# Kernel tuning notes

Measured on AMD Instinct MI355X. Metric: run time of the kernel, lower is better.

The kernel has to match this reference:

```python
import jax, jax.numpy as jnp
import numpy as np

T, B, D = 512, 32, 1024


def setup_inputs() -> dict:
    key = jax.random.key(0)
    kx, kwh, kwx, kwg = jax.random.split(key, 4)
    x = jax.random.normal(kx, (T, B, D), dtype=jnp.float32)
    # W_h: orthogonal init scaled by 0.5
    a = jax.random.normal(kwh, (D, D), dtype=jnp.float32)
    q, r = jnp.linalg.qr(a)
    W_h = 0.5 * q * jnp.sign(jnp.diag(r))[None, :]
    # xavier uniform for W_x, W_g: bound = sqrt(6/(D+D))
    bound = float(np.sqrt(6.0 / (D + D)))
    W_x = jax.random.uniform(kwx, (D, D), minval=-bound, maxval=bound, dtype=jnp.float32)
    W_g = jax.random.uniform(kwg, (D, D), minval=-bound, maxval=bound, dtype=jnp.float32)
    b = jnp.zeros((D,), dtype=jnp.float32)
    b_g = jnp.zeros((D,), dtype=jnp.float32)
    return {"x": x, "W_h": W_h, "W_x": W_x, "W_g": W_g, "b": b, "b_g": b_g}


def reference(x, W_h, W_x, W_g, b, b_g):
    # x: [T, B, D]
    Tn, Bn, Dn = x.shape
    # Precompute input projections (batched over T*B, like the torch code)
    Wx_all = jnp.einsum('tbd,ed->tbe', x, W_x)                      # [T,B,D]
    gate_all = jax.nn.sigmoid(jnp.einsum('tbd,ed->tbe', x, W_g) + b_g)  # [T,B,D]
    h0 = jnp.zeros((Bn, Dn), dtype=x.dtype)

    def step(h_prev, inp):
        wx_t, g_t = inp
        pre_act = h_prev @ W_h.T + wx_t + b
        h_new = h_prev + g_t * jnp.tanh(pre_act)
        out_t = h_new * jax.nn.silu(h_new)
        return h_new, (h_new, out_t)

    _, (h_seq, output) = jax.lax.scan(step, h0, (Wx_all, gate_all))
    h = jnp.concatenate([h0[None], h_seq], axis=0)  # [T+1,B,D]
    return output, h
```

## Files before the change

kernel.cpp:

```cpp
#include <hip/hip_runtime.h>
#include <hip/hip_bf16.h>
#include <stdint.h>


#define T_DIM 512
#define B_DIM 32
#define D_DIM 1024
#define M_DIM (T_DIM*B_DIM)
#define NANB 0x7FC00000u

typedef __attribute__((ext_vector_type(4))) float f32x4;
typedef __attribute__((ext_vector_type(4))) int   i32x4;
typedef __attribute__((ext_vector_type(8))) short bf16x8;

__device__ inline unsigned short f2b(float f){
  union { float f; uint32_t u; } c; c.f = f;
  uint32_t u = c.u + 0x7fffu + ((c.u >> 16) & 1u);
  return (unsigned short)(u >> 16);
}
__device__ inline float b2f(unsigned short h){
  union { uint32_t u; float f; } c; c.u = ((uint32_t)h) << 16;
  return c.f;
}

__global__ void init_kernel(float* __restrict__ out_h0, uint32_t* __restrict__ h_ex){
  int i = blockIdx.x*blockDim.x + threadIdx.x;
  if (i < 32768) out_h0[i] = 0.f;
  int slot = (i >> 12) & 15;
  h_ex[i] = (slot == 0) ? 0u : NANB;
}

template<int MODE>
__global__ __launch_bounds__(256, 2)
void proj_m(const float* __restrict__ X, const float* __restrict__ W,
            const float* __restrict__ bias, float* __restrict__ OUT)
{
  __shared__ unsigned short Ah[128*64];
  __shared__ unsigned short Al[128*64];
  __shared__ unsigned short Bh[128*64];
  __shared__ unsigned short Bl[128*64];
  char* AhB=(char*)Ah; char* AlB=(char*)Al; char* BhB=(char*)Bh; char* BlB=(char*)Bl;
  const int tid  = threadIdx.x;
  const int lane = tid & 63;
  const int wave = tid >> 6;
  const int m0 = blockIdx.y * 128;
  const int n0 = blockIdx.x * 128;
  const int wm = (wave >> 1) * 64;
  const int wn = (wave & 1) * 64;
  const int fr = lane & 15;
  const int fq = lane >> 4;

  f32x4 acc[4][4];
  #pragma unroll
  for (int i=0;i<4;++i)
    #pragma unroll
    for (int j=0;j<4;++j) acc[i][j] = (f32x4){0.f,0.f,0.f,0.f};

  for (int kt = 0; kt < D_DIM/64; ++kt) {
    #pragma unroll
    for (int c = 0; c < 4; ++c) {
      int idx = tid + c*256;
      int row = idx >> 3;
      int k8  = idx & 7;
      const float* ga = X + (size_t)(m0+row)*D_DIM + kt*64 + k8*8;
      const float* gb = W + (size_t)(n0+row)*D_DIM + kt*64 + k8*8;
      f32x4 a0 = *(const f32x4*)ga, a1 = *(const f32x4*)(ga+4);
      f32x4 b0 = *(const f32x4*)gb, b1 = *(const f32x4*)(gb+4);
      bf16x8 vah, val, vbh, vbl;
      #pragma unroll
      for (int j=0;j<4;++j){
        unsigned short h;
        h = f2b(a0[j]); vah[j]   = (short)h; val[j]   = (short)f2b(a0[j]-b2f(h));
        h = f2b(a1[j]); vah[4+j] = (short)h; val[4+j] = (short)f2b(a1[j]-b2f(h));
        h = f2b(b0[j]); vbh[j]   = (short)h; vbl[j]   = (short)f2b(b0[j]-b2f(h));
        h = f2b(b1[j]); vbh[4+j] = (short)h; vbl[4+j] = (short)f2b(b1[j]-b2f(h));
      }
      int lb = row*128 + ((k8*16) ^ ((row&7)<<4));
      *(bf16x8*)(AhB + lb) = vah;
      *(bf16x8*)(AlB + lb) = val;
      *(bf16x8*)(BhB + lb) = vbh;
      *(bf16x8*)(BlB + lb) = vbl;
    }
    __syncthreads();
    #pragma unroll
    for (int kk=0; kk<2; ++kk) {
      bf16x8 afh[4], afl[4], bfh[4], bfl[4];
      #pragma unroll
      for (int i=0;i<4;++i){
        int row = wm+i*16+fr;
        int off = row*128 + ((kk*64 + fq*16) ^ ((row&7)<<4));
        afh[i] = *(const bf16x8*)(AhB + off);
        afl[i] = *(const bf16x8*)(AlB + off);
      }
      #pragma unroll
      for (int j=0;j<4;++j){
        int row = wn+j*16+fr;
        int off = row*128 + ((kk*64 + fq*16) ^ ((row&7)<<4));
        bfh[j] = *(const bf16x8*)(BhB + off);
        bfl[j] = *(const bf16x8*)(BlB + off);
      }
      #pragma unroll
      for (int i=0;i<4;++i)
        #pragma unroll
        for (int j=0;j<4;++j){
          acc[i][j] = __builtin_amdgcn_mfma_f32_16x16x32_bf16(afh[i], bfh[j], acc[i][j], 0,0,0);
          acc[i][j] = __builtin_amdgcn_mfma_f32_16x16x32_bf16(afh[i], bfl[j], acc[i][j], 0,0,0);
          acc[i][j] = __builtin_amdgcn_mfma_f32_16x16x32_bf16(afl[i], bfh[j], acc[i][j], 0,0,0);
        }
    }
    __syncthreads();
  }
  #pragma unroll
  for (int j=0;j<4;++j) {
    int col = n0 + wn + j*16 + fr;
    float bv = bias[col];
    #pragma unroll
    for (int i=0;i<4;++i) {
      int rowb = m0 + wm + i*16 + fq*4;
      #pragma unroll
      for (int r=0;r<4;++r) {
        float v = acc[i][j][r] + bv;
        if (MODE==1) v = 1.f/(1.f + expf(-v));
        OUT[(size_t)(rowb+r)*D_DIM + col] = v;
      }
    }
  }
}

__global__ __launch_bounds__(256, 1)
void rnn_persist(const float* __restrict__ Wh,
                 float* PO,
                 float* PH,
                 float* __restrict__ h_ex)
{
  __shared__ char  hsb[4*4096];
  __shared__ float part[16*137];

  const int tid = threadIdx.x;
  const int blk = blockIdx.x;
  const int g   = blk & 7;
  const int sl  = blk >> 3;
  const int e0  = sl * 32;
  const int b0  = g * 4;
  const int e2  = tid & 15;
  const int kc  = tid >> 4;

  f32x4 wh0[16], wh1[16];
  {
    const f32x4* wp0 = (const f32x4*)(Wh + (size_t)(e0 + 2*e2 + 0)*D_DIM + kc*64);
    const f32x4* wp1 = (const f32x4*)(Wh + (size_t)(e0 + 2*e2 + 1)*D_DIM + kc*64);
    #pragma unroll
    for (int i = 0; i < 16; ++i) { wh0[i] = wp0[i]; wh1[i] = wp1[i]; }
  }

  const int bl = tid >> 5;
  const int el = tid & 31;
  float hold = 0.f;

  float Pv = 0.f, Gv = 0.f;
  if (tid < 128) {
    size_t idx0 = (size_t)(b0 + bl)*D_DIM + e0 + el;
    Pv = PH[idx0 + 32768];
    Gv = PO[idx0];
  }

  for (int t = 0; t < T_DIM; ++t) {
    size_t idx_out = (size_t)t*32768 + (size_t)(b0 + bl)*D_DIM + e0 + el;

    {
      const char* hsrc = (const char*)(h_ex + ((size_t)g*16 + (t & 15))*4096) + tid*16;
      i32x4 r0, r1, r2, r3;
      while (true) {
        asm volatile("global_load_dwordx4 %0, %1, off sc1" : "=v"(r0) : "v"(hsrc)         : "memory");
        asm volatile("global_load_dwordx4 %0, %1, off sc1" : "=v"(r1) : "v"(hsrc + 4096)  : "memory");
        asm volatile("global_load_dwordx4 %0, %1, off sc1" : "=v"(r2) : "v"(hsrc + 8192)  : "memory");
        asm volatile("global_load_dwordx4 %0, %1, off sc1" : "=v"(r3) : "v"(hsrc + 12288) : "memory");
        asm volatile("s_waitcnt vmcnt(0)" ::: "memory");
        __builtin_amdgcn_sched_barrier(0);
        bool ok = (r0[0]!=(int)NANB) & (r0[1]!=(int)NANB) & (r0[2]!=(int)NANB) & (r0[3]!=(int)NANB)
                & (r1[0]!=(int)NANB) & (r1[1]!=(int)NANB) & (r1[2]!=(int)NANB) & (r1[3]!=(int)NANB)
                & (r2[0]!=(int)NANB) & (r2[1]!=(int)NANB) & (r2[2]!=(int)NANB) & (r2[3]!=(int)NANB)
                & (r3[0]!=(int)NANB) & (r3[1]!=(int)NANB) & (r3[2]!=(int)NANB) & (r3[3]!=(int)NANB);
        if (ok) break;
        __builtin_amdgcn_s_sleep(2);
      }
      #pragma unroll
      for (int i = 0; i < 4; ++i) {
        int g16s = tid ^ (tid >> 4);
        i32x4 v = (i==0) ? r0 : (i==1) ? r1 : (i==2) ? r2 : r3;
        *(i32x4*)(hsb + i*4096 + g16s*16) = v;
      }
    }
    __syncthreads();

    float Pn = 0.f, Gn = 0.f;
    if (t + 1 < T_DIM && tid < 128) {
      size_t idx_n = (size_t)(t+1)*32768 + (size_t)(b0 + bl)*D_DIM + e0 + el;
      Pn = PH[idx_n + 32768];
      Gn = PO[idx_n];
    }

    float acc[4][2];
    #pragma unroll
    for (int b = 0; b < 4; ++b) { acc[b][0] = 0.f; acc[b][1] = 0.f; }
    #pragma unroll
    for (int i = 0; i < 16; ++i) {
      f32x4 w0 = wh0[i], w1 = wh1[i];
      #pragma unroll
      for (int b = 0; b < 4; ++b) {
        f32x4 hv = *(const f32x4*)(hsb + b*4096 + kc*256 + ((i ^ kc) << 4));
        float d0 = hv[0]*w0[0] + hv[1]*w0[1] + hv[2]*w0[2] + hv[3]*w0[3];
        float d1 = hv[0]*w1[0] + hv[1]*w1[1] + hv[2]*w1[2] + hv[3]*w1[3];
        acc[b][0] += d0;
        acc[b][1] += d1;
      }
    }
    #pragma unroll
    for (int b = 0; b < 4; ++b) {
      part[kc*137 + b*32 + 2*e2 + 0] = acc[b][0];
      part[kc*137 + b*32 + 2*e2 + 1] = acc[b][1];
    }
    __syncthreads();

    if (tid < 128) {
      float pre = 0.f;
      #pragma unroll
      for (int q = 0; q < 16; ++q) pre += part[q*137 + bl*32 + el];
      pre += Pv;
      float th = tanhf(pre);
      float hn = hold + Gv*th;
      hold = hn;
      float sg = 1.f/(1.f + expf(-hn));
      float* hdst = h_ex + ((size_t)g*16 + ((t+1) & 15))*4096 + (size_t)bl*1024 + e0 + el;
      asm volatile("global_store_dword %0, %1, off sc1" :: "v"(hdst), "v"(hn) : "memory");
      uint32_t nanb = NANB;
      float* ndst = h_ex + ((size_t)g*16 + ((t+9) & 15))*4096 + (size_t)bl*1024 + e0 + el;
      asm volatile("global_store_dword %0, %1, off sc1" :: "v"(ndst), "v"(nanb) : "memory");
      PH[idx_out + 32768] = hn;
      PO[idx_out] = hn*hn*sg;
    }
    Pv = Pn; Gv = Gn;
  }
}

extern "C" void kernel_launch(void* const* d_in, const int* in_sizes, int n_in,
                              void* d_out, int out_size, void* d_ws, size_t ws_size,
                              hipStream_t stream) {
  const float* x  = (const float*)d_in[0];
  const float* Wh = (const float*)d_in[1];
  const float* Wx = (const float*)d_in[2];
  const float* Wg = (const float*)d_in[3];
  const float* b  = (const float*)d_in[4];
  const float* bg = (const float*)d_in[5];

  float* out_o = (float*)d_out;
  float* out_h = out_o + (size_t)M_DIM*D_DIM;

  float* h_ex = (float*)d_ws;

  init_kernel<<<2048, 256, 0, stream>>>(out_h, (uint32_t*)h_ex);
  proj_m<1><<<dim3(8,128), 256, 0, stream>>>(x, Wg, bg, out_o);
  proj_m<0><<<dim3(8,128), 256, 0, stream>>>(x, Wx, b,  out_h + 32768);
  rnn_persist<<<256, 256, 0, stream>>>(Wh, out_o, out_h, h_ex);
}
```

Baseline: 1.649 ms.

## Split recurrent step into critical-path and side-work warp groups

Threads 0-127 now do the whole spin-poll of the exchanged hidden state, with twice as many loads each, plus the recurrence update and the h exchange store. Threads 128-255 prefetch the next step's P and G values into shared memory, compute the SiLU output, write PO/PH, and store the NaN poison marker. This takes the global output stores, the sigmoid and the next-step loads off the latency-critical warps. The cost is an extra __syncthreads per timestep and less parallelism in the poll loop.

```diff
diff --git a/kernel.cpp b/kernel.cpp
--- a/kernel.cpp
+++ b/kernel.cpp
@@ -135,6 +135,9 @@
 {
   __shared__ char  hsb[4*4096];
   __shared__ float part[16*137];
+  __shared__ float hout[128];
+  __shared__ float Pbuf[128];
+  __shared__ float Gbuf[128];
 
   const int tid = threadIdx.x;
   const int blk = blockIdx.x;
@@ -155,50 +158,62 @@
 
   const int bl = tid >> 5;
   const int el = tid & 31;
+  const int j2 = tid - 128;
+  const int bl2 = (j2 >> 5) & 3;
+  const int el2 = j2 & 31;
   float hold = 0.f;
 
-  float Pv = 0.f, Gv = 0.f;
-  if (tid < 128) {
-    size_t idx0 = (size_t)(b0 + bl)*D_DIM + e0 + el;
-    Pv = PH[idx0 + 32768];
-    Gv = PO[idx0];
+  float Pld = 0.f, Gld = 0.f;
+  if (tid >= 128) {
+    size_t idx0 = (size_t)(b0 + bl2)*D_DIM + e0 + el2;
+    const float* pp = PH + idx0 + 32768;
+    const float* gp = PO + idx0;
+    asm volatile("global_load_dword %0, %1, off" : "=v"(Pld) : "v"(pp) : "memory");
+    asm volatile("global_load_dword %0, %1, off" : "=v"(Gld) : "v"(gp) : "memory");
   }
 
   for (int t = 0; t < T_DIM; ++t) {
-    size_t idx_out = (size_t)t*32768 + (size_t)(b0 + bl)*D_DIM + e0 + el;
-
-    {
+
+    if (tid < 128) {
       const char* hsrc = (const char*)(h_ex + ((size_t)g*16 + (t & 15))*4096) + tid*16;
-      i32x4 r0, r1, r2, r3;
+      i32x4 r0, r1, r2, r3, r4, r5, r6, r7;
       while (true) {
         asm volatile("global_load_dwordx4 %0, %1, off sc1" : "=v"(r0) : "v"(hsrc)         : "memory");
-        asm volatile("global_load_dwordx4 %0, %1, off sc1" : "=v"(r1) : "v"(hsrc + 4096)  : "memory");
-        asm volatile("global_load_dwordx4 %0, %1, off sc1" : "=v"(r2) : "v"(hsrc + 8192)  : "memory");
-        asm volatile("global_load_dwordx4 %0, %1, off sc1" : "=v"(r3) : "v"(hsrc + 12288) : "memory");
+        asm volatile("global_load_dwordx4 %0, %1, off sc1" : "=v"(r1) : "v"(hsrc + 2048)  : "memory");
+        asm volatile("global_load_dwordx4 %0, %1, off sc1" : "=v"(r2) : "v"(hsrc + 4096)  : "memory");
+        asm volatile("global_load_dwordx4 %0, %1, off sc1" : "=v"(r3) : "v"(hsrc + 6144)  : "memory");
+        asm volatile("global_load_dwordx4 %0, %1, off sc1" : "=v"(r4) : "v"(hsrc + 8192)  : "memory");
+        asm volatile("global_load_dwordx4 %0, %1, off sc1" : "=v"(r5) : "v"(hsrc + 10240) : "memory");
+        asm volatile("global_load_dwordx4 %0, %1, off sc1" : "=v"(r6) : "v"(hsrc + 12288) : "memory");
+        asm volatile("global_load_dwordx4 %0, %1, off sc1" : "=v"(r7) : "v"(hsrc + 14336) : "memory");
         asm volatile("s_waitcnt vmcnt(0)" ::: "memory");
         __builtin_amdgcn_sched_barrier(0);
-        bool ok = (r0[0]!=(int)NANB) & (r0[1]!=(int)NANB) & (r0[2]!=(int)NANB) & (r0[3]!=(int)NANB)
-                & (r1[0]!=(int)NANB) & (r1[1]!=(int)NANB) & (r1[2]!=(int)NANB) & (r1[3]!=(int)NANB)
-                & (r2[0]!=(int)NANB) & (r2[1]!=(int)NANB) & (r2[2]!=(int)NANB) & (r2[3]!=(int)NANB)
-                & (r3[0]!=(int)NANB) & (r3[1]!=(int)NANB) & (r3[2]!=(int)NANB) & (r3[3]!=(int)NANB);
+        bool ok = (r0[0]!=(int)NANB)&(r0[1]!=(int)NANB)&(r0[2]!=(int)NANB)&(r0[3]!=(int)NANB)
+                & (r1[0]!=(int)NANB)&(r1[1]!=(int)NANB)&(r1[2]!=(int)NANB)&(r1[3]!=(int)NANB)
+                & (r2[0]!=(int)NANB)&(r2[1]!=(int)NANB)&(r2[2]!=(int)NANB)&(r2[3]!=(int)NANB)
+                & (r3[0]!=(int)NANB)&(r3[1]!=(int)NANB)&(r3[2]!=(int)NANB)&(r3[3]!=(int)NANB)
+                & (r4[0]!=(int)NANB)&(r4[1]!=(int)NANB)&(r4[2]!=(int)NANB)&(r4[3]!=(int)NANB)
+                & (r5[0]!=(int)NANB)&(r5[1]!=(int)NANB)&(r5[2]!=(int)NANB)&(r5[3]!=(int)NANB)
+                & (r6[0]!=(int)NANB)&(r6[1]!=(int)NANB)&(r6[2]!=(int)NANB)&(r6[3]!=(int)NANB)
+                & (r7[0]!=(int)NANB)&(r7[1]!=(int)NANB)&(r7[2]!=(int)NANB)&(r7[3]!=(int)NANB);
         if (ok) break;
         __builtin_amdgcn_s_sleep(2);
       }
       #pragma unroll
-      for (int i = 0; i < 4; ++i) {
-        int g16s = tid ^ (tid >> 4);
-        i32x4 v = (i==0) ? r0 : (i==1) ? r1 : (i==2) ? r2 : r3;
-        *(i32x4*)(hsb + i*4096 + g16s*16) = v;
-      }
-    }
-    __syncthreads();
-
-    float Pn = 0.f, Gn = 0.f;
-    if (t + 1 < T_DIM && tid < 128) {
-      size_t idx_n = (size_t)(t+1)*32768 + (size_t)(b0 + bl)*D_DIM + e0 + el;
-      Pn = PH[idx_n + 32768];
-      Gn = PO[idx_n];
-    }
+      for (int l = 0; l < 8; ++l) {
+        int plane = l >> 1;
+        int g16   = tid + ((l & 1) << 7);
+        int g16s  = g16 ^ (g16 >> 4);
+        i32x4 v = (l==0)?r0:(l==1)?r1:(l==2)?r2:(l==3)?r3:(l==4)?r4:(l==5)?r5:(l==6)?r6:r7;
+        *(i32x4*)(hsb + plane*4096 + g16s*16) = v;
+      }
+    } else {
+      asm volatile("s_waitcnt vmcnt(0)" ::: "memory");
+      __builtin_amdgcn_sched_barrier(0);
+      Pbuf[j2] = Pld;
+      Gbuf[j2] = Gld;
+    }
+    __syncthreads();
 
     float acc[4][2];
     #pragma unroll
@@ -226,20 +241,33 @@
       float pre = 0.f;
       #pragma unroll
       for (int q = 0; q < 16; ++q) pre += part[q*137 + bl*32 + el];
-      pre += Pv;
+      pre += Pbuf[tid];
       float th = tanhf(pre);
-      float hn = hold + Gv*th;
+      float hn = hold + Gbuf[tid]*th;
       hold = hn;
-      float sg = 1.f/(1.f + expf(-hn));
       float* hdst = h_ex + ((size_t)g*16 + ((t+1) & 15))*4096 + (size_t)bl*1024 + e0 + el;
       asm volatile("global_store_dword %0, %1, off sc1" :: "v"(hdst), "v"(hn) : "memory");
+      hout[tid] = hn;
+    }
+    __syncthreads();
+
+    if (tid >= 128) {
+      float hn = hout[j2];
+      if (t + 1 < T_DIM) {
+        size_t idx_n = (size_t)(t+1)*32768 + (size_t)(b0 + bl2)*D_DIM + e0 + el2;
+        const float* pp = PH + idx_n + 32768;
+        const float* gp = PO + idx_n;
+        asm volatile("global_load_dword %0, %1, off" : "=v"(Pld) : "v"(pp) : "memory");
+        asm volatile("global_load_dword %0, %1, off" : "=v"(Gld) : "v"(gp) : "memory");
+      }
+      float sg = 1.f/(1.f + expf(-hn));
+      size_t idx2 = (size_t)t*32768 + (size_t)(b0 + bl2)*D_DIM + e0 + el2;
+      PO[idx2] = hn*hn*sg;
+      PH[idx2 + 32768] = hn;
       uint32_t nanb = NANB;
-      float* ndst = h_ex + ((size_t)g*16 + ((t+9) & 15))*4096 + (size_t)bl*1024 + e0 + el;
+      float* ndst = h_ex + ((size_t)g*16 + ((t+9) & 15))*4096 + (size_t)bl2*1024 + e0 + el2;
       asm volatile("global_store_dword %0, %1, off sc1" :: "v"(ndst), "v"(nanb) : "memory");
-      PH[idx_out + 32768] = hn;
-      PO[idx_out] = hn*hn*sg;
-    }
-    Pv = Pn; Gv = Gn;
+    }
   }
 }
 
```

Result: slower. 2.144 ms (+30.1%).
